# Kernel optimization log

Measured on AMD Instinct MI355X. Metric: run time of the kernel, lower is better.

Reference implementation:

```python
import jax, jax.numpy as jnp
from jax import lax
import numpy as np

WIN = 9          # window size per spatial dim (default [9]*ndims)
PAD = WIN // 2
EPS = 1e-07


def _box_sum(x, groups):
    # depthwise conv with all-ones kernel == sliding-window sum
    kernel = jnp.ones((groups, 1, WIN, WIN), dtype=x.dtype)
    return lax.conv_general_dilated(
        x, kernel,
        window_strides=(1, 1),
        padding=[(PAD, PAD), (PAD, PAD)],
        feature_group_count=groups,
        dimension_numbers=('NCHW', 'OIHW', 'NCHW'))


def setup_inputs() -> dict:
    key = jax.random.key(0)
    k1, k2 = jax.random.split(key)
    shape = (8, 1, 1024, 1024)
    y_pred = jax.random.normal(k1, shape, dtype=jnp.float32)
    y_true = jax.random.normal(k2, shape, dtype=jnp.float32)
    return {"y_pred": y_pred, "y_true": y_true}


def reference(y_pred, y_true):
    Ii = y_true
    Ji = y_pred
    groups = Ii.shape[1]
    win_size = float(WIN * WIN)

    I_sum = _box_sum(Ii, groups)
    J_sum = _box_sum(Ji, groups)
    I2_sum = _box_sum(Ii * Ii, groups)
    J2_sum = _box_sum(Ji * Ji, groups)
    IJ_sum = _box_sum(Ii * Ji, groups)

    u_I = I_sum / win_size
    u_J = J_sum / win_size
    cross = IJ_sum / win_size - u_I * u_J
    I_var = I2_sum / win_size - u_I * u_I
    J_var = J2_sum / win_size - u_J * u_J

    cc = cross / jnp.sqrt(jnp.maximum(I_var * J_var, EPS))
    return 1.0 - jnp.mean(cc)
```

## Files before the change

### kernel.cpp

```cpp
#include <hip/hip_runtime.h>

#define H 1024
#define W 1024
#define TY 16
#define NT 64
#define RS 10
#define NG 66
#define NBK 64

__global__ void ncc_zero(double* acc) {
    if (threadIdx.x < NBK) acc[threadIdx.x] = 0.0;
}

__global__ void ncc_finalize(const double* __restrict__ acc, float* __restrict__ out) {
    double s = 0.0;
    #pragma unroll
    for (int i = 0; i < NBK; ++i) s += acc[i];
    out[0] = 1.0f - (float)(s * (1.0 / 8388608.0));
}

__device__ __forceinline__ unsigned pk2(float lo, float hi) {
    unsigned r;
    asm("v_cvt_pk_bf16_f32 %0, %1, %2" : "=v"(r) : "v"(lo), "v"(hi));
    return r;
}
__device__ __forceinline__ float ulo(unsigned u) { return __uint_as_float(u << 16); }
__device__ __forceinline__ float uhi(unsigned u) { return __uint_as_float(u & 0xffff0000u); }

__global__ __launch_bounds__(NT) void ncc_main(
    const float* __restrict__ Jg,
    const float* __restrict__ Ig,
    double* __restrict__ acc)
{
    __shared__ uint4 ring[RS][NG];

    const int n     = blockIdx.x;
    const int b     = n & 7;
    const int rest  = n >> 3;
    const int panel = rest & 3;
    const int strip = rest >> 2;
    const int y0    = strip * TY;
    const int lane  = threadIdx.x;
    const int wb    = panel << 8;
    const int x0    = wb + (lane << 2);

    const float* __restrict__ Ib = Ig + (size_t)b * (H * W);
    const float* __restrict__ Jb = Jg + (size_t)b * (H * W);

    const bool  hl  = (lane < 2);
    const int   hx  = (lane == 0) ? (wb - 4) : (wb + 256);
    const float mhx = (hl && (unsigned)hx <= (unsigned)(W - 4)) ? 1.0f : 0.0f;
    const int   hxc = min(max(hx, 0), W - 4);
    const int   hg  = (lane == 0) ? 0 : (NG - 1);

    float rI[4]={0,0,0,0}, rJ[4]={0,0,0,0}, rII[4]={0,0,0,0}, rJJ[4]={0,0,0,0}, rIJ[4]={0,0,0,0};
    float accv = 0.0f;
    const float inv = 1.0f / 81.0f;

    float4 Pi, Pj, Phi = {0,0,0,0}, Phj = {0,0,0,0};
    float  Pm;

#define FLOAD(yy) do {                                                              \
        const int r_ = (yy);                                                        \
        Pm = ((unsigned)r_ < (unsigned)H) ? 1.0f : 0.0f;                            \
        const int rc_ = min(max(r_, 0), H - 1);                                     \
        Pi = *(const float4*)(Ib + (size_t)rc_ * W + x0);                           \
        Pj = *(const float4*)(Jb + (size_t)rc_ * W + x0);                           \
        if (hl) {                                                                   \
            Phi = *(const float4*)(Ib + (size_t)rc_ * W + hxc);                     \
            Phj = *(const float4*)(Jb + (size_t)rc_ * W + hxc);                     \
        }                                                                           \
    } while (0)

#define PACKW(sl) do {                                                              \
        uint4 v_;                                                                   \
        v_.x = pk2(Pi.x * Pm, Pi.y * Pm);                                           \
        v_.y = pk2(Pi.z * Pm, Pi.w * Pm);                                           \
        v_.z = pk2(Pj.x * Pm, Pj.y * Pm);                                           \
        v_.w = pk2(Pj.z * Pm, Pj.w * Pm);                                           \
        ring[sl][lane + 1] = v_;                                                    \
        if (hl) {                                                                   \
            const float mm_ = Pm * mhx;                                             \
            uint4 h_;                                                               \
            h_.x = pk2(Phi.x * mm_, Phi.y * mm_);                                   \
            h_.y = pk2(Phi.z * mm_, Phi.w * mm_);                                   \
            h_.z = pk2(Phj.x * mm_, Phj.y * mm_);                                   \
            h_.w = pk2(Phj.z * mm_, Phj.w * mm_);                                   \
            ring[sl][hg] = h_;                                                      \
        }                                                                           \
    } while (0)

#define READS(sl, G0, G1, G2) do {                                                  \
        G0 = ring[sl][lane];                                                        \
        G1 = ring[sl][lane + 1];                                                    \
        G2 = ring[sl][lane + 2];                                                    \
    } while (0)

#define FOLD12(G0, G1, G2, SG) do {                                                 \
        const float i0=ulo(G0.x), i1=uhi(G0.x), i2=ulo(G0.y), i3=uhi(G0.y);         \
        const float i4=ulo(G1.x), i5=uhi(G1.x), i6=ulo(G1.y), i7=uhi(G1.y);         \
        const float i8=ulo(G2.x), i9=uhi(G2.x), i10=ulo(G2.y), i11=uhi(G2.y);       \
        const float j0=ulo(G0.z), j1=uhi(G0.z), j2=ulo(G0.w), j3=uhi(G0.w);         \
        const float j4=ulo(G1.z), j5=uhi(G1.z), j6=ulo(G1.w), j7=uhi(G1.w);         \
        const float j8=ulo(G2.z), j9=uhi(G2.z), j10=ulo(G2.w), j11=uhi(G2.w);       \
        { float s_ = i0+i1+i2+i3+i4+i5+i6+i7+i8;                                    \
          rI[0] += SG*s_; s_ += i9-i0;  rI[1] += SG*s_;                             \
          s_ += i10-i1;   rI[2] += SG*s_; s_ += i11-i2; rI[3] += SG*s_; }           \
        { float s_ = j0+j1+j2+j3+j4+j5+j6+j7+j8;                                    \
          rJ[0] += SG*s_; s_ += j9-j0;  rJ[1] += SG*s_;                             \
          s_ += j10-j1;   rJ[2] += SG*s_; s_ += j11-j2; rJ[3] += SG*s_; }           \
        { const float q0=i0*i0,q1=i1*i1,q2=i2*i2,q3=i3*i3,q4=i4*i4,q5=i5*i5;        \
          const float q6=i6*i6,q7=i7*i7,q8=i8*i8,q9=i9*i9,q10=i10*i10,q11=i11*i11;  \
          float s_ = q0+q1+q2+q3+q4+q5+q6+q7+q8;                                    \
          rII[0] += SG*s_; s_ += q9-q0;  rII[1] += SG*s_;                           \
          s_ += q10-q1;    rII[2] += SG*s_; s_ += q11-q2; rII[3] += SG*s_; }        \
        { const float q0=j0*j0,q1=j1*j1,q2=j2*j2,q3=j3*j3,q4=j4*j4,q5=j5*j5;        \
          const float q6=j6*j6,q7=j7*j7,q8=j8*j8,q9=j9*j9,q10=j10*j10,q11=j11*j11;  \
          float s_ = q0+q1+q2+q3+q4+q5+q6+q7+q8;                                    \
          rJJ[0] += SG*s_; s_ += q9-q0;  rJJ[1] += SG*s_;                           \
          s_ += q10-q1;    rJJ[2] += SG*s_; s_ += q11-q2; rJJ[3] += SG*s_; }        \
        { const float q0=i0*j0,q1=i1*j1,q2=i2*j2,q3=i3*j3,q4=i4*j4,q5=i5*j5;        \
          const float q6=i6*j6,q7=i7*j7,q8=i8*j8,q9=i9*j9,q10=i10*j10,q11=i11*j11;  \
          float s_ = q0+q1+q2+q3+q4+q5+q6+q7+q8;                                    \
          rIJ[0] += SG*s_; s_ += q9-q0;  rIJ[1] += SG*s_;                           \
          s_ += q10-q1;    rIJ[2] += SG*s_; s_ += q11-q2; rIJ[3] += SG*s_; }        \
    } while (0)

#define CC() do {                                                                   \
        _Pragma("unroll")                                                           \
        for (int c = 0; c < 4; ++c) {                                               \
            const float uI    = rI[c] * inv;                                        \
            const float uJ    = rJ[c] * inv;                                        \
            const float cross = rIJ[c] * inv - uI * uJ;                             \
            const float Iv    = rII[c] * inv - uI * uI;                             \
            const float Jv    = rJJ[c] * inv - uJ * uJ;                             \
            accv += cross * rsqrtf(fmaxf(Iv * Jv, 1e-7f));                          \
        }                                                                           \
    } while (0)

    FLOAD(y0 - 4);
    #pragma unroll 1
    for (int r = 0; r < 9; ++r) {
        PACKW(r);
        asm volatile("" ::: "memory");
        uint4 G0, G1, G2;
        READS(r, G0, G1, G2);
        asm volatile("" ::: "memory");
        FLOAD(y0 - 3 + r);
        FOLD12(G0, G1, G2, 1.0f);
    }

    int ls = 0, es = 9;
    #pragma unroll 1
    for (int k = 0; k < TY - 1; ++k) {
        PACKW(es);
        asm volatile("" ::: "memory");
        uint4 e0, e1, e2, l0, l1, l2;
        READS(es, e0, e1, e2);
        READS(ls, l0, l1, l2);
        asm volatile("" ::: "memory");
        FLOAD(y0 + 6 + k);
        CC();
        FOLD12(e0, e1, e2,  1.0f);
        FOLD12(l0, l1, l2, -1.0f);
        ls = (ls == RS - 1) ? 0 : ls + 1;
        es = (es == RS - 1) ? 0 : es + 1;
    }
    CC();

#undef CC
#undef FOLD12
#undef READS
#undef PACKW
#undef FLOAD

    #pragma unroll
    for (int off = 32; off > 0; off >>= 1)
        accv += __shfl_down(accv, off);
    if (lane == 0)
        atomicAdd(&acc[n & (NBK - 1)], (double)accv);
}

extern "C" void kernel_launch(void* const* d_in, const int* in_sizes, int n_in,
                              void* d_out, int out_size, void* d_ws, size_t ws_size,
                              hipStream_t stream) {
    const float* y_pred = (const float*)d_in[0];
    const float* y_true = (const float*)d_in[1];
    float* out = (float*)d_out;
    double* accp = (double*)d_ws;

    ncc_zero<<<dim3(1), dim3(NBK), 0, stream>>>(accp);
    ncc_main<<<dim3(8 * 4 * (H / TY)), dim3(NT), 0, stream>>>(y_pred, y_true, accp);
    ncc_finalize<<<dim3(1), dim3(1), 0, stream>>>(accp, out);
}
```

Baseline: 43.64 us.

## Reorder separable box filter to vertical-first running sums with LDS horizontal pass

Swaps the order of the separable 9x9 box sum. Each thread now keeps per-column vertical running sums of I, J, I², J², IJ and publishes them to a shared-memory row buffer. A horizontal 9-tap sliding sum is then taken from neighbouring columns, and halo lanes maintain the edge columns. This removes the redundant 12-element horizontal folds done twice per row, cutting ALU work. In exchange it adds shared-memory writes and reads of float sums every row, plus extra halo bookkeeping in divergent lanes.

```diff
diff --git a/kernel.cpp b/kernel.cpp
--- a/kernel.cpp
+++ b/kernel.cpp
@@ -6,6 +6,7 @@
 #define NT 64
 #define RS 10
 #define NG 66
+#define LW 264
 #define NBK 64
 
 __global__ void ncc_zero(double* acc) {
@@ -33,6 +34,7 @@
     double* __restrict__ acc)
 {
     __shared__ uint4 ring[RS][NG];
+    __shared__ float vs[5][LW];
 
     const int n     = blockIdx.x;
     const int b     = n & 7;
@@ -43,17 +45,24 @@
     const int lane  = threadIdx.x;
     const int wb    = panel << 8;
     const int x0    = wb + (lane << 2);
+    const int xw    = lane << 2;
 
     const float* __restrict__ Ib = Ig + (size_t)b * (H * W);
     const float* __restrict__ Jb = Jg + (size_t)b * (H * W);
 
-    const bool  hl  = (lane < 2);
+    const bool  hw  = (lane < 2);
     const int   hx  = (lane == 0) ? (wb - 4) : (wb + 256);
-    const float mhx = (hl && (unsigned)hx <= (unsigned)(W - 4)) ? 1.0f : 0.0f;
+    const float mhx = (hw && (unsigned)hx <= (unsigned)(W - 4)) ? 1.0f : 0.0f;
     const int   hxc = min(max(hx, 0), W - 4);
-    const int   hg  = (lane == 0) ? 0 : (NG - 1);
-
-    float rI[4]={0,0,0,0}, rJ[4]={0,0,0,0}, rII[4]={0,0,0,0}, rJJ[4]={0,0,0,0}, rIJ[4]={0,0,0,0};
+    const int   hgw = (lane == 0) ? 0 : (NG - 1);
+
+    const bool  isH   = (lane < 8);
+    const int   hg8   = (lane < 4) ? 0 : (NG - 1);
+    const int   hidx  = lane & 3;
+    const int   hslot = (lane < 4) ? lane : (256 + lane);
+
+    float sI[4]={0,0,0,0}, sJ[4]={0,0,0,0}, sII[4]={0,0,0,0}, sJJ[4]={0,0,0,0}, sIJ[4]={0,0,0,0};
+    float hs0=0, hs1=0, hs2=0, hs3=0, hs4=0;
     float accv = 0.0f;
     const float inv = 1.0f / 81.0f;
 
@@ -66,111 +75,135 @@
         const int rc_ = min(max(r_, 0), H - 1);                                     \
         Pi = *(const float4*)(Ib + (size_t)rc_ * W + x0);                           \
         Pj = *(const float4*)(Jb + (size_t)rc_ * W + x0);                           \
-        if (hl) {                                                                   \
+        if (hw) {                                                                   \
             Phi = *(const float4*)(Ib + (size_t)rc_ * W + hxc);                     \
             Phj = *(const float4*)(Jb + (size_t)rc_ * W + hxc);                     \
         }                                                                           \
     } while (0)
 
 #define PACKW(sl) do {                                                              \
-        uint4 v_;                                                                   \
-        v_.x = pk2(Pi.x * Pm, Pi.y * Pm);                                           \
-        v_.y = pk2(Pi.z * Pm, Pi.w * Pm);                                           \
-        v_.z = pk2(Pj.x * Pm, Pj.y * Pm);                                           \
-        v_.w = pk2(Pj.z * Pm, Pj.w * Pm);                                           \
-        ring[sl][lane + 1] = v_;                                                    \
-        if (hl) {                                                                   \
+        pkv.x = pk2(Pi.x * Pm, Pi.y * Pm);                                          \
+        pkv.y = pk2(Pi.z * Pm, Pi.w * Pm);                                          \
+        pkv.z = pk2(Pj.x * Pm, Pj.y * Pm);                                          \
+        pkv.w = pk2(Pj.z * Pm, Pj.w * Pm);                                          \
+        ring[sl][lane + 1] = pkv;                                                   \
+        if (hw) {                                                                   \
             const float mm_ = Pm * mhx;                                             \
             uint4 h_;                                                               \
             h_.x = pk2(Phi.x * mm_, Phi.y * mm_);                                   \
             h_.y = pk2(Phi.z * mm_, Phi.w * mm_);                                   \
             h_.z = pk2(Phj.x * mm_, Phj.y * mm_);                                   \
             h_.w = pk2(Phj.z * mm_, Phj.w * mm_);                                   \
-            ring[sl][hg] = h_;                                                      \
+            ring[sl][hgw] = h_;                                                     \
         }                                                                           \
     } while (0)
 
-#define READS(sl, G0, G1, G2) do {                                                  \
-        G0 = ring[sl][lane];                                                        \
-        G1 = ring[sl][lane + 1];                                                    \
-        G2 = ring[sl][lane + 2];                                                    \
-    } while (0)
-
-#define FOLD12(G0, G1, G2, SG) do {                                                 \
-        const float i0=ulo(G0.x), i1=uhi(G0.x), i2=ulo(G0.y), i3=uhi(G0.y);         \
-        const float i4=ulo(G1.x), i5=uhi(G1.x), i6=ulo(G1.y), i7=uhi(G1.y);         \
-        const float i8=ulo(G2.x), i9=uhi(G2.x), i10=ulo(G2.y), i11=uhi(G2.y);       \
-        const float j0=ulo(G0.z), j1=uhi(G0.z), j2=ulo(G0.w), j3=uhi(G0.w);         \
-        const float j4=ulo(G1.z), j5=uhi(G1.z), j6=ulo(G1.w), j7=uhi(G1.w);         \
-        const float j8=ulo(G2.z), j9=uhi(G2.z), j10=ulo(G2.w), j11=uhi(G2.w);       \
-        { float s_ = i0+i1+i2+i3+i4+i5+i6+i7+i8;                                    \
-          rI[0] += SG*s_; s_ += i9-i0;  rI[1] += SG*s_;                             \
-          s_ += i10-i1;   rI[2] += SG*s_; s_ += i11-i2; rI[3] += SG*s_; }           \
-        { float s_ = j0+j1+j2+j3+j4+j5+j6+j7+j8;                                    \
-          rJ[0] += SG*s_; s_ += j9-j0;  rJ[1] += SG*s_;                             \
-          s_ += j10-j1;   rJ[2] += SG*s_; s_ += j11-j2; rJ[3] += SG*s_; }           \
-        { const float q0=i0*i0,q1=i1*i1,q2=i2*i2,q3=i3*i3,q4=i4*i4,q5=i5*i5;        \
-          const float q6=i6*i6,q7=i7*i7,q8=i8*i8,q9=i9*i9,q10=i10*i10,q11=i11*i11;  \
-          float s_ = q0+q1+q2+q3+q4+q5+q6+q7+q8;                                    \
-          rII[0] += SG*s_; s_ += q9-q0;  rII[1] += SG*s_;                           \
-          s_ += q10-q1;    rII[2] += SG*s_; s_ += q11-q2; rII[3] += SG*s_; }        \
-        { const float q0=j0*j0,q1=j1*j1,q2=j2*j2,q3=j3*j3,q4=j4*j4,q5=j5*j5;        \
-          const float q6=j6*j6,q7=j7*j7,q8=j8*j8,q9=j9*j9,q10=j10*j10,q11=j11*j11;  \
-          float s_ = q0+q1+q2+q3+q4+q5+q6+q7+q8;                                    \
-          rJJ[0] += SG*s_; s_ += q9-q0;  rJJ[1] += SG*s_;                           \
-          s_ += q10-q1;    rJJ[2] += SG*s_; s_ += q11-q2; rJJ[3] += SG*s_; }        \
-        { const float q0=i0*j0,q1=i1*j1,q2=i2*j2,q3=i3*j3,q4=i4*j4,q5=i5*j5;        \
-          const float q6=i6*j6,q7=i7*j7,q8=i8*j8,q9=i9*j9,q10=i10*j10,q11=i11*j11;  \
-          float s_ = q0+q1+q2+q3+q4+q5+q6+q7+q8;                                    \
-          rIJ[0] += SG*s_; s_ += q9-q0;  rIJ[1] += SG*s_;                           \
-          s_ += q10-q1;    rIJ[2] += SG*s_; s_ += q11-q2; rIJ[3] += SG*s_; }        \
-    } while (0)
-
-#define CC() do {                                                                   \
-        _Pragma("unroll")                                                           \
-        for (int c = 0; c < 4; ++c) {                                               \
-            const float uI    = rI[c] * inv;                                        \
-            const float uJ    = rJ[c] * inv;                                        \
-            const float cross = rIJ[c] * inv - uI * uJ;                             \
-            const float Iv    = rII[c] * inv - uI * uI;                             \
-            const float Jv    = rJJ[c] * inv - uJ * uJ;                             \
-            accv += cross * rsqrtf(fmaxf(Iv * Jv, 1e-7f));                          \
+#define FOLDOWN(G, SG) do {                                                         \
+        const float i0=ulo(G.x), i1=uhi(G.x), i2=ulo(G.y), i3=uhi(G.y);             \
+        const float j0=ulo(G.z), j1=uhi(G.z), j2=ulo(G.w), j3=uhi(G.w);             \
+        sI[0]+=SG*i0; sI[1]+=SG*i1; sI[2]+=SG*i2; sI[3]+=SG*i3;                     \
+        sJ[0]+=SG*j0; sJ[1]+=SG*j1; sJ[2]+=SG*j2; sJ[3]+=SG*j3;                     \
+        sII[0]+=SG*i0*i0; sII[1]+=SG*i1*i1; sII[2]+=SG*i2*i2; sII[3]+=SG*i3*i3;     \
+        sJJ[0]+=SG*j0*j0; sJJ[1]+=SG*j1*j1; sJJ[2]+=SG*j2*j2; sJJ[3]+=SG*j3*j3;     \
+        sIJ[0]+=SG*i0*j0; sIJ[1]+=SG*i1*j1; sIJ[2]+=SG*i2*j2; sIJ[3]+=SG*i3*j3;     \
+    } while (0)
+
+#define FOLDHALO(G, SG) do {                                                        \
+        const unsigned ui_ = (hidx < 2) ? G.x : G.y;                                \
+        const unsigned uj_ = (hidx < 2) ? G.z : G.w;                                \
+        const float iv_ = (hidx & 1) ? uhi(ui_) : ulo(ui_);                         \
+        const float jv_ = (hidx & 1) ? uhi(uj_) : ulo(uj_);                         \
+        hs0 += SG*iv_; hs1 += SG*jv_;                                               \
+        hs2 += SG*iv_*iv_; hs3 += SG*jv_*jv_; hs4 += SG*iv_*jv_;                    \
+    } while (0)
+
+#define PUB() do {                                                                  \
+        *(float4*)&vs[0][4 + xw] = make_float4(sI[0],  sI[1],  sI[2],  sI[3]);      \
+        *(float4*)&vs[1][4 + xw] = make_float4(sJ[0],  sJ[1],  sJ[2],  sJ[3]);      \
+        *(float4*)&vs[2][4 + xw] = make_float4(sII[0], sII[1], sII[2], sII[3]);     \
+        *(float4*)&vs[3][4 + xw] = make_float4(sJJ[0], sJJ[1], sJJ[2], sJJ[3]);     \
+        *(float4*)&vs[4][4 + xw] = make_float4(sIJ[0], sIJ[1], sIJ[2], sIJ[3]);     \
+        if (isH) {                                                                  \
+            vs[0][hslot] = hs0; vs[1][hslot] = hs1; vs[2][hslot] = hs2;             \
+            vs[3][hslot] = hs3; vs[4][hslot] = hs4;                                 \
         }                                                                           \
+    } while (0)
+
+#define HTAP(a, cg, T, o) do {                                                      \
+        float s_ = a.x + a.y + a.z + a.w + cg.x + T;                                \
+        o[0] = s_; s_ += cg.y - a.x;                                                \
+        o[1] = s_; s_ += cg.z - a.y;                                                \
+        o[2] = s_; s_ += cg.w - a.z;                                                \
+        o[3] = s_;                                                                  \
     } while (0)
 
     FLOAD(y0 - 4);
     #pragma unroll 1
     for (int r = 0; r < 9; ++r) {
+        uint4 pkv;
         PACKW(r);
         asm volatile("" ::: "memory");
-        uint4 G0, G1, G2;
-        READS(r, G0, G1, G2);
+        uint4 he = make_uint4(0, 0, 0, 0);
+        if (isH) he = ring[r][hg8];
         asm volatile("" ::: "memory");
         FLOAD(y0 - 3 + r);
-        FOLD12(G0, G1, G2, 1.0f);
+        FOLDOWN(pkv, 1.0f);
+        if (isH) FOLDHALO(he, 1.0f);
     }
 
     int ls = 0, es = 9;
     #pragma unroll 1
-    for (int k = 0; k < TY - 1; ++k) {
+    for (int k = 0; k < TY; ++k) {
+        PUB();
+        asm volatile("" ::: "memory");
+        float4 a0 = *(const float4*)&vs[0][xw], c0 = *(const float4*)&vs[0][xw + 8];
+        float4 a1 = *(const float4*)&vs[1][xw], c1 = *(const float4*)&vs[1][xw + 8];
+        float4 a2 = *(const float4*)&vs[2][xw], c2 = *(const float4*)&vs[2][xw + 8];
+        float4 a3 = *(const float4*)&vs[3][xw], c3 = *(const float4*)&vs[3][xw + 8];
+        float4 a4 = *(const float4*)&vs[4][xw], c4 = *(const float4*)&vs[4][xw + 8];
+        asm volatile("" ::: "memory");
+
+        const float T0 = sI[0]  + sI[1]  + sI[2]  + sI[3];
+        const float T1 = sJ[0]  + sJ[1]  + sJ[2]  + sJ[3];
+        const float T2 = sII[0] + sII[1] + sII[2] + sII[3];
+        const float T3 = sJJ[0] + sJJ[1] + sJJ[2] + sJJ[3];
+        const float T4 = sIJ[0] + sIJ[1] + sIJ[2] + sIJ[3];
+
+        uint4 pkv;
         PACKW(es);
         asm volatile("" ::: "memory");
-        uint4 e0, e1, e2, l0, l1, l2;
-        READS(es, e0, e1, e2);
-        READS(ls, l0, l1, l2);
-        asm volatile("" ::: "memory");
+        uint4 lv = ring[ls][lane + 1];
+        uint4 he = make_uint4(0, 0, 0, 0), hl = make_uint4(0, 0, 0, 0);
+        if (isH) { he = ring[es][hg8]; hl = ring[ls][hg8]; }
+        asm volatile("" ::: "memory");
+
         FLOAD(y0 + 6 + k);
-        CC();
-        FOLD12(e0, e1, e2,  1.0f);
-        FOLD12(l0, l1, l2, -1.0f);
+
+        float h0[4], h1[4], h2[4], h3[4], h4[4];
+        HTAP(a0, c0, T0, h0); HTAP(a1, c1, T1, h1); HTAP(a2, c2, T2, h2);
+        HTAP(a3, c3, T3, h3); HTAP(a4, c4, T4, h4);
+        #pragma unroll
+        for (int c = 0; c < 4; ++c) {
+            const float uI    = h0[c] * inv;
+            const float uJ    = h1[c] * inv;
+            const float cross = h4[c] * inv - uI * uJ;
+            const float Iv    = h2[c] * inv - uI * uI;
+            const float Jv    = h3[c] * inv - uJ * uJ;
+            accv += cross * rsqrtf(fmaxf(Iv * Jv, 1e-7f));
+        }
+
+        FOLDOWN(pkv, 1.0f);
+        FOLDOWN(lv, -1.0f);
+        if (isH) { FOLDHALO(he, 1.0f); FOLDHALO(hl, -1.0f); }
+
         ls = (ls == RS - 1) ? 0 : ls + 1;
         es = (es == RS - 1) ? 0 : es + 1;
     }
-    CC();
-
-#undef CC
-#undef FOLD12
-#undef READS
+
+#undef HTAP
+#undef PUB
+#undef FOLDHALO
+#undef FOLDOWN
 #undef PACKW
 #undef FLOAD
 
```

Measured after the change: 37.21 us, median of 2. 1.17x faster.
